# Kernel tuning notes

Measured on AMD Instinct MI355X. Metric: run time of the kernel, lower is better.

Reference implementation:

```python
import jax, jax.numpy as jnp
import numpy as np

BATCH = 4096
N_AG = 32       # nodes (agents) per batch element
N_HE = 8        # hyperedges per batch element
F_IN = 256
F_OUT = 128
N_NODES = BATCH * N_AG
N_EDGES = BATCH * N_HE


def _build_incidence():
    # dense per-batch incidence (randn hyper_graph => all entries nonzero),
    # block-diagonal across the batch via index offsets
    b = jnp.arange(BATCH, dtype=jnp.int32)
    nodes = b[:, None, None] * N_AG + jnp.arange(N_AG, dtype=jnp.int32)[None, :, None]
    edges = b[:, None, None] * N_HE + jnp.arange(N_HE, dtype=jnp.int32)[None, None, :]
    node_idx = jnp.broadcast_to(nodes, (BATCH, N_AG, N_HE)).reshape(-1)
    edge_idx = jnp.broadcast_to(edges, (BATCH, N_AG, N_HE)).reshape(-1)
    return node_idx, edge_idx


def setup_inputs() -> dict:
    key = jax.random.key(0)
    k1, k2, k3 = jax.random.split(key, 3)
    inp = jax.random.normal(k1, (BATCH, N_AG, F_IN), jnp.float32)
    lin_w = jax.random.normal(k2, (F_IN, F_OUT), jnp.float32) * (1.0 / np.sqrt(F_IN))
    hgcn_bias = jnp.zeros((F_OUT,), jnp.float32)
    out_w = jax.random.normal(k3, (F_OUT, F_OUT), jnp.float32) * (1.0 / np.sqrt(F_OUT))
    out_b = jnp.zeros((F_OUT,), jnp.float32)
    node_idx, edge_idx = _build_incidence()
    return {"input": inp, "lin_w": lin_w, "hgcn_bias": hgcn_bias,
            "out_w": out_w, "out_b": out_b,
            "node_idx": node_idx, "edge_idx": edge_idx}


def reference(input, lin_w, hgcn_bias, out_w, out_b, node_idx, edge_idx):
    # X' = D^-1 H B^-1 H^T X Theta + bias, then Linear+ReLU output layer
    x = input.reshape(-1, F_IN) @ lin_w                       # [N, F_OUT]
    w = jnp.ones((N_EDGES,), x.dtype)                         # default hyperedge weights
    # node degree D (weighted by hyperedge weight) and edge degree B
    D = jax.ops.segment_sum(w[edge_idx], node_idx, num_segments=N_NODES)
    D_inv = jnp.where(D > 0, 1.0 / D, 0.0)
    deg = jax.ops.segment_sum(jnp.ones(edge_idx.shape, x.dtype), edge_idx,
                              num_segments=N_EDGES)
    B_inv = jnp.where(deg > 0, 1.0 / deg, 0.0)
    # propagate nodes -> hyperedges with norm B^-1 at target edges
    edge_feat = jax.ops.segment_sum(x[node_idx] * B_inv[edge_idx][:, None],
                                    edge_idx, num_segments=N_EDGES)   # [M, F_OUT]
    # propagate hyperedges -> nodes with norm D^-1 at target nodes
    out = jax.ops.segment_sum(edge_feat[edge_idx] * D_inv[node_idx][:, None],
                              node_idx, num_segments=N_NODES)         # [N, F_OUT]
    out = out + hgcn_bias
    return jax.nn.relu(out @ out_w + out_b)
```

## Files before the change

### kernel.cpp

```cpp
#include <hip/hip_runtime.h>


constexpr int BATCH = 4096;
constexpr int N_AG  = 32;
constexpr int F_IN  = 256;
constexpr int F_OUT = 128;
constexpr int G     = 4;

typedef float vfloat4 __attribute__((ext_vector_type(4)));

__global__ __launch_bounds__(256, 4) void hgcn_fused(
    const float* __restrict__ input,
    const float* __restrict__ lin_w,
    const float* __restrict__ bias1,
    const float* __restrict__ out_w,
    const float* __restrict__ bias2,
    float* __restrict__ out)
{
    const int t  = threadIdx.x;
    const int b0 = blockIdx.x * G;

    __shared__ __align__(16) float m[G][F_IN];
    __shared__ __align__(16) float part[2][G][F_OUT];
    __shared__ __align__(16) float h[G][F_OUT];
    __shared__ __align__(16) float y[G][F_OUT];

    const int j    = t & 127;
    const int half = t >> 7;
    const int gs   = t >> 7;

    {
        const int g  = t >> 6;
        const int f4 = t & 63;
        const vfloat4* in4 = (const vfloat4*)input + (size_t)(b0 + g) * (N_AG * F_IN / 4);
        vfloat4 s = (vfloat4)0.f;
        #pragma unroll
        for (int a = 0; a < N_AG; ++a) {
            vfloat4 v = __builtin_nontemporal_load(&in4[a * (F_IN / 4) + f4]);
            s += v;
        }
        s *= (1.0f / 32.0f);
        *(vfloat4*)&m[g][f4 * 4] = s;
    }
    __syncthreads();

    {
        float acc[G] = {0.f, 0.f, 0.f, 0.f};
        const int fbase = half * (F_IN / 2);
        #pragma unroll 4
        for (int fi = 0; fi < F_IN / 2; ++fi) {
            const int f = fbase + fi;
            const float w = lin_w[f * F_OUT + j];
            #pragma unroll
            for (int g = 0; g < G; ++g) acc[g] += m[g][f] * w;
        }
        #pragma unroll
        for (int g = 0; g < G; ++g) part[half][g][j] = acc[g];
    }
    __syncthreads();
    {
        const float bb = bias1[j];
        #pragma unroll
        for (int gg = gs; gg < G; gg += 2)
            h[gg][j] = part[0][gg][j] + part[1][gg][j] + bb;
    }
    __syncthreads();

    {
        float acc[G] = {0.f, 0.f, 0.f, 0.f};
        const int kbase = half * (F_OUT / 2);
        #pragma unroll 4
        for (int ki = 0; ki < F_OUT / 2; ++ki) {
            const int k = kbase + ki;
            const float w = out_w[k * F_OUT + j];
            #pragma unroll
            for (int g = 0; g < G; ++g) acc[g] += h[g][k] * w;
        }
        #pragma unroll
        for (int g = 0; g < G; ++g) part[half][g][j] = acc[g];
    }
    __syncthreads();
    {
        const float bb = bias2[j];
        #pragma unroll
        for (int gg = gs; gg < G; gg += 2) {
            const float v = part[0][gg][j] + part[1][gg][j] + bb;
            y[gg][j] = v > 0.f ? v : 0.f;
        }
    }
    __syncthreads();

    {
        vfloat4* o4 = (vfloat4*)out + (size_t)b0 * (N_AG * F_OUT / 4);
        const vfloat4* y4 = (const vfloat4*)&y[0][0];
        const int col = t & 31;
        vfloat4 vy[G];
        #pragma unroll
        for (int g = 0; g < G; ++g) vy[g] = y4[g * 32 + col];
        #pragma unroll
        for (int r = 0; r < 16; ++r) {
            const int i = r * 256 + t;
            __builtin_nontemporal_store(vy[r >> 2], &o4[i]);
        }
    }
}

extern "C" void kernel_launch(void* const* d_in, const int* in_sizes, int n_in,
                              void* d_out, int out_size, void* d_ws, size_t ws_size,
                              hipStream_t stream) {
    const float* input = (const float*)d_in[0];
    const float* lin_w = (const float*)d_in[1];
    const float* b1    = (const float*)d_in[2];
    const float* out_w = (const float*)d_in[3];
    const float* b2    = (const float*)d_in[4];
    float* out = (float*)d_out;

    hgcn_fused<<<BATCH / G, 256, 0, stream>>>(input, lin_w, b1, out_w, b2, out);
}
```

Before: 222.9 us.

## Assign one wavefront per batch element and remove block barriers

```diff
diff --git a/kernel.cpp b/kernel.cpp
--- a/kernel.cpp
+++ b/kernel.cpp
@@ -5,9 +5,10 @@
 constexpr int N_AG  = 32;
 constexpr int F_IN  = 256;
 constexpr int F_OUT = 128;
-constexpr int G     = 4;
+constexpr int WPB   = 4;
 
 typedef float vfloat4 __attribute__((ext_vector_type(4)));
+typedef float vfloat2 __attribute__((ext_vector_type(2)));
 
 __global__ __launch_bounds__(256, 4) void hgcn_fused(
     const float* __restrict__ input,
@@ -17,90 +18,76 @@
     const float* __restrict__ bias2,
     float* __restrict__ out)
 {
-    const int t  = threadIdx.x;
-    const int b0 = blockIdx.x * G;
+    const int t    = threadIdx.x;
+    const int w    = t >> 6;
+    const int lane = t & 63;
+    const int b    = blockIdx.x * WPB + w;
 
-    __shared__ __align__(16) float m[G][F_IN];
-    __shared__ __align__(16) float part[2][G][F_OUT];
-    __shared__ __align__(16) float h[G][F_OUT];
-    __shared__ __align__(16) float y[G][F_OUT];
-
-    const int j    = t & 127;
-    const int half = t >> 7;
-    const int gs   = t >> 7;
+    __shared__ __align__(16) float sm[WPB][F_IN];
+    __shared__ __align__(16) float sh[WPB][F_OUT];
+    __shared__ __align__(16) float sy[WPB][F_OUT];
 
     {
-        const int g  = t >> 6;
-        const int f4 = t & 63;
-        const vfloat4* in4 = (const vfloat4*)input + (size_t)(b0 + g) * (N_AG * F_IN / 4);
+        const vfloat4* in4 = (const vfloat4*)input + (size_t)b * (N_AG * F_IN / 4);
         vfloat4 s = (vfloat4)0.f;
         #pragma unroll
-        for (int a = 0; a < N_AG; ++a) {
-            vfloat4 v = __builtin_nontemporal_load(&in4[a * (F_IN / 4) + f4]);
-            s += v;
-        }
+        for (int a = 0; a < N_AG; ++a)
+            s += __builtin_nontemporal_load(&in4[a * (F_IN / 4) + lane]);
         s *= (1.0f / 32.0f);
-        *(vfloat4*)&m[g][f4 * 4] = s;
+        *(vfloat4*)&sm[w][lane * 4] = s;
     }
-    __syncthreads();
 
     {
-        float acc[G] = {0.f, 0.f, 0.f, 0.f};
-        const int fbase = half * (F_IN / 2);
+        const vfloat2* lw2 = (const vfloat2*)lin_w;
+        const vfloat4* m4  = (const vfloat4*)&sm[w][0];
+        float a0 = 0.f, a1 = 0.f;
         #pragma unroll 4
-        for (int fi = 0; fi < F_IN / 2; ++fi) {
-            const int f = fbase + fi;
-            const float w = lin_w[f * F_OUT + j];
+        for (int f4 = 0; f4 < F_IN / 4; ++f4) {
+            vfloat4 mm = m4[f4];
             #pragma unroll
-            for (int g = 0; g < G; ++g) acc[g] += m[g][f] * w;
+            for (int c = 0; c < 4; ++c) {
+                vfloat2 wv = lw2[(f4 * 4 + c) * (F_OUT / 2) + lane];
+                a0 += mm[c] * wv.x;
+                a1 += mm[c] * wv.y;
+            }
         }
-        #pragma unroll
-        for (int g = 0; g < G; ++g) part[half][g][j] = acc[g];
+        vfloat2 bb = ((const vfloat2*)bias1)[lane];
+        vfloat2 hv; hv.x = a0 + bb.x; hv.y = a1 + bb.y;
+        *(vfloat2*)&sh[w][lane * 2] = hv;
     }
-    __syncthreads();
-    {
-        const float bb = bias1[j];
-        #pragma unroll
-        for (int gg = gs; gg < G; gg += 2)
-            h[gg][j] = part[0][gg][j] + part[1][gg][j] + bb;
-    }
-    __syncthreads();
 
     {
-        float acc[G] = {0.f, 0.f, 0.f, 0.f};
-        const int kbase = half * (F_OUT / 2);
+        const vfloat2* ow2 = (const vfloat2*)out_w;
+        const vfloat4* h4  = (const vfloat4*)&sh[w][0];
+        float a0 = 0.f, a1 = 0.f;
         #pragma unroll 4
-        for (int ki = 0; ki < F_OUT / 2; ++ki) {
-            const int k = kbase + ki;
-            const float w = out_w[k * F_OUT + j];
+        for (int k4 = 0; k4 < F_OUT / 4; ++k4) {
+            vfloat4 hh = h4[k4];
             #pragma unroll
-            for (int g = 0; g < G; ++g) acc[g] += h[g][k] * w;
+            for (int c = 0; c < 4; ++c) {
+                vfloat2 wv = ow2[(k4 * 4 + c) * (F_OUT / 2) + lane];
+                a0 += hh[c] * wv.x;
+                a1 += hh[c] * wv.y;
+            }
         }
-        #pragma unroll
-        for (int g = 0; g < G; ++g) part[half][g][j] = acc[g];
+        vfloat2 bb = ((const vfloat2*)bias2)[lane];
+        float y0 = a0 + bb.x, y1 = a1 + bb.y;
+        vfloat2 yv;
+        yv.x = y0 > 0.f ? y0 : 0.f;
+        yv.y = y1 > 0.f ? y1 : 0.f;
+        *(vfloat2*)&sy[w][lane * 2] = yv;
     }
-    __syncthreads();
-    {
-        const float bb = bias2[j];
-        #pragma unroll
-        for (int gg = gs; gg < G; gg += 2) {
-            const float v = part[0][gg][j] + part[1][gg][j] + bb;
-            y[gg][j] = v > 0.f ? v : 0.f;
-        }
-    }
-    __syncthreads();
 
     {
-        vfloat4* o4 = (vfloat4*)out + (size_t)b0 * (N_AG * F_OUT / 4);
-        const vfloat4* y4 = (const vfloat4*)&y[0][0];
-        const int col = t & 31;
-        vfloat4 vy[G];
+        const vfloat4* y4 = (const vfloat4*)&sy[w][0];
+        const int col  = lane & 31;
+        const int half = lane >> 5;
+        vfloat4 vy = y4[col];
+        vfloat4* o4 = (vfloat4*)out + (size_t)b * (N_AG * F_OUT / 4);
         #pragma unroll
-        for (int g = 0; g < G; ++g) vy[g] = y4[g * 32 + col];
-        #pragma unroll
-        for (int r = 0; r < 16; ++r) {
-            const int i = r * 256 + t;
-            __builtin_nontemporal_store(vy[r >> 2], &o4[i]);
+        for (int r2 = 0; r2 < 16; ++r2) {
+            const int row = r2 * 2 + half;
+            __builtin_nontemporal_store(vy, &o4[row * (F_OUT / 4) + col]);
         }
     }
 }
@@ -115,5 +102,5 @@
     const float* b2    = (const float*)d_in[4];
     float* out = (float*)d_out;
 
-    hgcn_fused<<<BATCH / G, 256, 0, stream>>>(input, lin_w, b1, out_w, b2, out);
+    hgcn_fused<<<BATCH / WPB, 256, 0, stream>>>(input, lin_w, b1, out_w, b2, out);
 }
```

Measured after the change: 245.5 us. +10.2%, slower.

## Process eight batches per block with 512 threads and vectorized split-K GEMVs

Applied to the files above, without the earlier changes.

```diff
diff --git a/kernel.cpp b/kernel.cpp
--- a/kernel.cpp
+++ b/kernel.cpp
@@ -5,11 +5,12 @@
 constexpr int N_AG  = 32;
 constexpr int F_IN  = 256;
 constexpr int F_OUT = 128;
-constexpr int G     = 4;
+constexpr int G     = 8;
 
 typedef float vfloat4 __attribute__((ext_vector_type(4)));
+typedef float vfloat2 __attribute__((ext_vector_type(2)));
 
-__global__ __launch_bounds__(256, 4) void hgcn_fused(
+__global__ __launch_bounds__(512, 4) void hgcn_fused(
     const float* __restrict__ input,
     const float* __restrict__ lin_w,
     const float* __restrict__ bias1,
@@ -20,14 +21,13 @@
     const int t  = threadIdx.x;
     const int b0 = blockIdx.x * G;
 
-    __shared__ __align__(16) float m[G][F_IN];
-    __shared__ __align__(16) float part[2][G][F_OUT];
-    __shared__ __align__(16) float h[G][F_OUT];
-    __shared__ __align__(16) float y[G][F_OUT];
+    __shared__ __align__(16) float sm[G][F_IN];
+    __shared__ __align__(16) float part[8][G][F_OUT];
+    __shared__ __align__(16) float sh[G][F_OUT];
+    __shared__ __align__(16) float sy[G][F_OUT];
 
-    const int j    = t & 127;
-    const int half = t >> 7;
-    const int gs   = t >> 7;
+    const int j2  = t & 63;
+    const int oct = t >> 6;
 
     {
         const int g  = t >> 6;
@@ -35,72 +35,111 @@
         const vfloat4* in4 = (const vfloat4*)input + (size_t)(b0 + g) * (N_AG * F_IN / 4);
         vfloat4 s = (vfloat4)0.f;
         #pragma unroll
-        for (int a = 0; a < N_AG; ++a) {
-            vfloat4 v = __builtin_nontemporal_load(&in4[a * (F_IN / 4) + f4]);
-            s += v;
-        }
+        for (int a = 0; a < N_AG; ++a)
+            s += __builtin_nontemporal_load(&in4[a * (F_IN / 4) + f4]);
         s *= (1.0f / 32.0f);
-        *(vfloat4*)&m[g][f4 * 4] = s;
+        *(vfloat4*)&sm[g][f4 * 4] = s;
     }
     __syncthreads();
 
     {
-        float acc[G] = {0.f, 0.f, 0.f, 0.f};
-        const int fbase = half * (F_IN / 2);
-        #pragma unroll 4
-        for (int fi = 0; fi < F_IN / 2; ++fi) {
-            const int f = fbase + fi;
-            const float w = lin_w[f * F_OUT + j];
+        const vfloat2* lw2 = (const vfloat2*)lin_w;
+        const vfloat4* m4  = (const vfloat4*)&sm[0][0];
+        vfloat2 acc[G];
+        #pragma unroll
+        for (int g = 0; g < G; ++g) acc[g] = (vfloat2)0.f;
+        #pragma unroll 2
+        for (int f4 = 0; f4 < 8; ++f4) {
+            vfloat4 mm[G];
             #pragma unroll
-            for (int g = 0; g < G; ++g) acc[g] += m[g][f] * w;
+            for (int g = 0; g < G; ++g)
+                mm[g] = m4[g * (F_IN / 4) + oct * 8 + f4];
+            #pragma unroll
+            for (int c = 0; c < 4; ++c) {
+                const int f = oct * 32 + f4 * 4 + c;
+                vfloat2 wv = lw2[f * (F_OUT / 2) + j2];
+                #pragma unroll
+                for (int g = 0; g < G; ++g) {
+                    acc[g].x += mm[g][c] * wv.x;
+                    acc[g].y += mm[g][c] * wv.y;
+                }
+            }
         }
         #pragma unroll
-        for (int g = 0; g < G; ++g) part[half][g][j] = acc[g];
-    }
-    __syncthreads();
-    {
-        const float bb = bias1[j];
-        #pragma unroll
-        for (int gg = gs; gg < G; gg += 2)
-            h[gg][j] = part[0][gg][j] + part[1][gg][j] + bb;
+        for (int g = 0; g < G; ++g)
+            *(vfloat2*)&part[oct][g][j2 * 2] = acc[g];
     }
     __syncthreads();
 
     {
-        float acc[G] = {0.f, 0.f, 0.f, 0.f};
-        const int kbase = half * (F_OUT / 2);
-        #pragma unroll 4
-        for (int ki = 0; ki < F_OUT / 2; ++ki) {
-            const int k = kbase + ki;
-            const float w = out_w[k * F_OUT + j];
-            #pragma unroll
-            for (int g = 0; g < G; ++g) acc[g] += h[g][k] * w;
-        }
+        const int g = t >> 6;
+        const vfloat2* p2 = (const vfloat2*)&part[0][0][0];
+        vfloat2 s = (vfloat2)0.f;
         #pragma unroll
-        for (int g = 0; g < G; ++g) part[half][g][j] = acc[g];
-    }
-    __syncthreads();
-    {
-        const float bb = bias2[j];
-        #pragma unroll
-        for (int gg = gs; gg < G; gg += 2) {
-            const float v = part[0][gg][j] + part[1][gg][j] + bb;
-            y[gg][j] = v > 0.f ? v : 0.f;
-        }
+        for (int o = 0; o < 8; ++o)
+            s += p2[(o * G + g) * (F_OUT / 2) + j2];
+        vfloat2 bb = ((const vfloat2*)bias1)[j2];
+        s += bb;
+        *(vfloat2*)&sh[g][j2 * 2] = s;
     }
     __syncthreads();
 
     {
-        vfloat4* o4 = (vfloat4*)out + (size_t)b0 * (N_AG * F_OUT / 4);
-        const vfloat4* y4 = (const vfloat4*)&y[0][0];
+        const vfloat2* ow2 = (const vfloat2*)out_w;
+        const vfloat4* h4  = (const vfloat4*)&sh[0][0];
+        vfloat2 acc[G];
+        #pragma unroll
+        for (int g = 0; g < G; ++g) acc[g] = (vfloat2)0.f;
+        #pragma unroll 2
+        for (int k4 = 0; k4 < 4; ++k4) {
+            vfloat4 hh[G];
+            #pragma unroll
+            for (int g = 0; g < G; ++g)
+                hh[g] = h4[g * (F_OUT / 4) + oct * 4 + k4];
+            #pragma unroll
+            for (int c = 0; c < 4; ++c) {
+                const int k = oct * 16 + k4 * 4 + c;
+                vfloat2 wv = ow2[k * (F_OUT / 2) + j2];
+                #pragma unroll
+                for (int g = 0; g < G; ++g) {
+                    acc[g].x += hh[g][c] * wv.x;
+                    acc[g].y += hh[g][c] * wv.y;
+                }
+            }
+        }
+        #pragma unroll
+        for (int g = 0; g < G; ++g)
+            *(vfloat2*)&part[oct][g][j2 * 2] = acc[g];
+    }
+    __syncthreads();
+
+    {
+        const int g = t >> 6;
+        const vfloat2* p2 = (const vfloat2*)&part[0][0][0];
+        vfloat2 s = (vfloat2)0.f;
+        #pragma unroll
+        for (int o = 0; o < 8; ++o)
+            s += p2[(o * G + g) * (F_OUT / 2) + j2];
+        vfloat2 bb = ((const vfloat2*)bias2)[j2];
+        s += bb;
+        vfloat2 yv;
+        yv.x = s.x > 0.f ? s.x : 0.f;
+        yv.y = s.y > 0.f ? s.y : 0.f;
+        *(vfloat2*)&sy[g][j2 * 2] = yv;
+    }
+    __syncthreads();
+
+    {
+        const vfloat4* y4 = (const vfloat4*)&sy[0][0];
         const int col = t & 31;
         vfloat4 vy[G];
         #pragma unroll
         for (int g = 0; g < G; ++g) vy[g] = y4[g * 32 + col];
+        vfloat4* o4 = (vfloat4*)out + (size_t)b0 * (N_AG * F_OUT / 4);
         #pragma unroll
         for (int r = 0; r < 16; ++r) {
-            const int i = r * 256 + t;
-            __builtin_nontemporal_store(vy[r >> 2], &o4[i]);
+            const int i = r * 512 + t;
+            __builtin_nontemporal_store(vy[r >> 1], &o4[i]);
         }
     }
 }
@@ -115,5 +154,5 @@
     const float* b2    = (const float*)d_in[4];
     float* out = (float*)d_out;
 
-    hgcn_fused<<<BATCH / G, 256, 0, stream>>>(input, lin_w, b1, out_w, b2, out);
+    hgcn_fused<<<BATCH / G, 512, 0, stream>>>(input, lin_w, b1, out_w, b2, out);
 }
```

Result: faster. 214.8 us (-3.6%).
